# Performance work log

Hardware: AMD Instinct MI355X
Metric: run time of the kernel (lower is better)

## Reference

```python
import jax, jax.numpy as jnp
import numpy as np

H = 2048          # hidden_size
NH = 16           # num_heads
HD = H // NH      # head_dim = 128
B, S = 2, 2048


def setup_inputs() -> dict:
    key = jax.random.key(0)
    ks = jax.random.split(key, 9)
    sc_h = 1.0 / np.sqrt(H)
    x = jax.random.normal(ks[0], (B, S, H), dtype=jnp.float32)
    # torch nn.Linear weights are [out_features, in_features]
    Wq = jax.random.uniform(ks[1], (H, H), jnp.float32, -sc_h, sc_h)
    bq = jax.random.uniform(ks[2], (H,), jnp.float32, -sc_h, sc_h)
    Wk = jax.random.uniform(ks[3], (HD, H), jnp.float32, -sc_h, sc_h)
    bk = jax.random.uniform(ks[4], (HD,), jnp.float32, -sc_h, sc_h)
    Wv = jax.random.uniform(ks[5], (HD, H), jnp.float32, -sc_h, sc_h)
    bv = jax.random.uniform(ks[6], (HD,), jnp.float32, -sc_h, sc_h)
    Wo = jax.random.uniform(ks[7], (H, H), jnp.float32, -sc_h, sc_h)
    bo = jax.random.uniform(ks[8], (H,), jnp.float32, -sc_h, sc_h)
    return {"x": x, "Wq": Wq, "bq": bq, "Wk": Wk, "bk": bk,
            "Wv": Wv, "bv": bv, "Wo": Wo, "bo": bo}


def reference(x, Wq, bq, Wk, bk, Wv, bv, Wo, bo):
    b, s, _ = x.shape
    q = (jnp.einsum('bsh,oh->bso', x, Wq) + bq).reshape(b, s, NH, HD)
    q = q.transpose(0, 2, 1, 3)                      # [b, nh, s, hd]
    k = jnp.einsum('bsh,dh->bsd', x, Wk) + bk        # [b, s, hd] single KV head
    v = jnp.einsum('bsh,dh->bsd', x, Wv) + bv
    # shared-K attention scores: broadcast single K head across query heads
    attn = jnp.einsum('bnsd,btd->bnst', q, k) / jnp.sqrt(jnp.float32(HD))
    attn = jax.nn.softmax(attn, axis=-1)
    out = jnp.einsum('bnst,btd->bnsd', attn, v)      # [b, nh, s, hd]
    out = out.transpose(0, 2, 1, 3).reshape(b, s, H)
    return jnp.einsum('bsh,oh->bso', out, Wo) + bo
```

## Files before the change

### kernel.cpp

```cpp
#include <hip/hip_runtime.h>
#include <hip/hip_bf16.h>

typedef unsigned short u16;
typedef unsigned int u32;
typedef __bf16 bf16x8 __attribute__((ext_vector_type(8)));
typedef float f32x4 __attribute__((ext_vector_type(4)));

#define AS1 __attribute__((address_space(1)))
#define AS3 __attribute__((address_space(3)))

__device__ __forceinline__ u16 f2bf(float f) {
  unsigned u = __builtin_bit_cast(unsigned, f);
  u += 0x7FFFu + ((u >> 16) & 1u);
  return (u16)(u >> 16);
}

__device__ __forceinline__ void gload_lds16(const void* g, void* l) {
  __builtin_amdgcn_global_load_lds((AS1 void*)g, (AS3 void*)l, 16, 0, 0);
}

__global__ __launch_bounds__(256)
void cvt_all(const float* __restrict__ x,
             const float* __restrict__ Wq, const float* __restrict__ Wk,
             const float* __restrict__ Wv, const float* __restrict__ Wo,
             const float* __restrict__ bq, const float* __restrict__ bk,
             const float* __restrict__ bv,
             u16* __restrict__ xb, u16* __restrict__ wqkv, u16* __restrict__ wo,
             float* __restrict__ bias_a, float qs) {
  const long NX = 1048576, NQ = 524288, NK = 32768, NV = 32768, NO = 524288;
  const long NW = NX + NQ + NK + NV + NO;
  long i = (long)blockIdx.x * 256 + threadIdx.x;
  if (i >= NW) {
    int t = (int)(i - NW);
    if (t < 2048) bias_a[t] = bq[t] * qs;
    else if (t < 2176) bias_a[t] = bk[t - 2048];
    else if (t < 2304) bias_a[t] = bv[t - 2176];
    return;
  }
  const float* src;
  u16* dst;
  float s = 1.f;
  if (i < NX) { src = x + i * 8; dst = xb + i * 8; }
  else if (i < NX + NQ) { long j = i - NX; src = Wq + j * 8; dst = wqkv + j * 8; s = qs; }
  else if (i < NX + NQ + NK) { long j = i - NX - NQ; src = Wk + j * 8; dst = wqkv + 2048l * 2048 + j * 8; }
  else if (i < NX + NQ + NK + NV) { long j = i - NX - NQ - NK; src = Wv + j * 8; dst = wqkv + 2176l * 2048 + j * 8; }
  else { long j = i - NX - NQ - NK - NV; src = Wo + j * 8; dst = wo + j * 8; }
  float4 a = *(const float4*)src;
  float4 b = *(const float4*)(src + 4);
  u16 t[8] = {f2bf(a.x * s), f2bf(a.y * s), f2bf(a.z * s), f2bf(a.w * s),
              f2bf(b.x * s), f2bf(b.y * s), f2bf(b.z * s), f2bf(b.w * s)};
  *(uint4*)dst = *(const uint4*)t;
}

__global__ __launch_bounds__(256)
void gemm_qkv(const u16* __restrict__ A, const u16* __restrict__ B,
              const float* __restrict__ bias, u16* __restrict__ Cq,
              u16* __restrict__ Ck, u16* __restrict__ Cvt, int K)
{
  __shared__ u16 As[128 * 64];
  __shared__ u16 Bs[128 * 64];
  const int tid = threadIdx.x;
  const int wave = tid >> 6, lane = tid & 63;
  const int g = lane >> 4, r = lane & 15;
  const int wrow = (wave >> 1) * 64, wcol = (wave & 1) * 64;

  const int gx = gridDim.x;
  int lin = blockIdx.y * gx + blockIdx.x;
  const int cpx = (gx * gridDim.y) >> 3;
  lin = (lin & 7) * cpx + (lin >> 3);
  const long tM = (long)(lin / gx) * 128, tN = (long)(lin % gx) * 128;

  const int srow = (tid * 16) >> 7;
  const int scol = (tid & 7) * 8;

  f32x4 acc[4][4] = {};
  char* As3 = (char*)As;
  char* Bs3 = (char*)Bs;

  for (int kt = 0; kt < K; kt += 64) {
    __syncthreads();
#pragma unroll
    for (int p = 0; p < 4; p++) {
      const int row = p * 32 + srow;
      const int sc = scol ^ ((row & 7) << 3);
      gload_lds16(A + (tM + row) * K + kt + sc, As3 + p * 4096 + tid * 16);
      gload_lds16(B + (tN + row) * K + kt + sc, Bs3 + p * 4096 + tid * 16);
    }
    __syncthreads();

#pragma unroll
    for (int kk = 0; kk < 2; kk++) {
      bf16x8 a[4], b[4];
#pragma unroll
      for (int m = 0; m < 4; m++) {
        const int ra = wrow + m * 16 + r;
        a[m] = *(const bf16x8*)(As + ra * 64 + ((kk * 32 + g * 8) ^ ((ra & 7) << 3)));
      }
#pragma unroll
      for (int n = 0; n < 4; n++) {
        const int rb = wcol + n * 16 + r;
        b[n] = *(const bf16x8*)(Bs + rb * 64 + ((kk * 32 + g * 8) ^ ((rb & 7) << 3)));
      }
#pragma unroll
      for (int m = 0; m < 4; m++)
#pragma unroll
        for (int n = 0; n < 4; n++)
          acc[m][n] = __builtin_amdgcn_mfma_f32_16x16x32_bf16(a[m], b[n], acc[m][n], 0, 0, 0);
    }
  }

#pragma unroll
  for (int m = 0; m < 4; m++) {
    const long row0 = tM + wrow + m * 16 + g * 4;
#pragma unroll
    for (int n = 0; n < 4; n++) {
      const long col = tN + wcol + n * 16 + r;
      const float bb = bias[col];
      u16 vals[4];
#pragma unroll
      for (int q = 0; q < 4; q++) vals[q] = f2bf(acc[m][n][q] + bb);
      if (col < 2048) {
#pragma unroll
        for (int q = 0; q < 4; q++)
          Cq[(row0 + q) * 2048 + col] = vals[q];
      } else if (col < 2176) {
#pragma unroll
        for (int q = 0; q < 4; q++)
          Ck[(row0 + q) * 128 + (col - 2048)] = vals[q];
      } else {
        const long b2 = row0 >> 11;
        const long t0r = row0 & 2047;
        const int tl = (int)(t0r & 63);
        const int base = ((tl >> 5) & 1) * 32 + ((tl >> 2) & 3) * 8 + ((tl >> 4) & 1) * 4;
        u16* vp = Cvt + (b2 * 128 + (col - 2176)) * 2048 + (t0r >> 6) * 64;
        *(ushort4*)(vp + base) = *(const ushort4*)vals;
      }
    }
  }
}

__global__ __launch_bounds__(256)
void gemm_out(const u16* __restrict__ A, const u16* __restrict__ B,
              const float* __restrict__ bias, float* __restrict__ C,
              int N, int K)
{
  __shared__ u16 As[128 * 64];
  __shared__ u16 Bs[128 * 64];
  const int tid = threadIdx.x;
  const int wave = tid >> 6, lane = tid & 63;
  const int g = lane >> 4, r = lane & 15;
  const int wrow = (wave >> 1) * 64, wcol = (wave & 1) * 64;

  const int gx = gridDim.x;
  int lin = blockIdx.y * gx + blockIdx.x;
  const int cpx = (gx * gridDim.y) >> 3;
  lin = (lin & 7) * cpx + (lin >> 3);
  const long tM = (long)(lin / gx) * 128, tN = (long)(lin % gx) * 128;

  const int srow = (tid * 16) >> 7;
  const int scol = (tid & 7) * 8;

  f32x4 acc[4][4] = {};
  char* As3 = (char*)As;
  char* Bs3 = (char*)Bs;

  for (int kt = 0; kt < K; kt += 64) {
    __syncthreads();
#pragma unroll
    for (int p = 0; p < 4; p++) {
      const int row = p * 32 + srow;
      const int sc = scol ^ ((row & 7) << 3);
      gload_lds16(A + (tM + row) * K + kt + sc, As3 + p * 4096 + tid * 16);
      gload_lds16(B + (tN + row) * K + kt + sc, Bs3 + p * 4096 + tid * 16);
    }
    __syncthreads();

#pragma unroll
    for (int kk = 0; kk < 2; kk++) {
      bf16x8 a[4], b[4];
#pragma unroll
      for (int m = 0; m < 4; m++) {
        const int ra = wrow + m * 16 + r;
        a[m] = *(const bf16x8*)(As + ra * 64 + ((kk * 32 + g * 8) ^ ((ra & 7) << 3)));
      }
#pragma unroll
      for (int n = 0; n < 4; n++) {
        const int rb = wcol + n * 16 + r;
        b[n] = *(const bf16x8*)(Bs + rb * 64 + ((kk * 32 + g * 8) ^ ((rb & 7) << 3)));
      }
#pragma unroll
      for (int m = 0; m < 4; m++)
#pragma unroll
        for (int n = 0; n < 4; n++)
          acc[m][n] = __builtin_amdgcn_mfma_f32_16x16x32_bf16(a[m], b[n], acc[m][n], 0, 0, 0);
    }
  }

#pragma unroll
  for (int m = 0; m < 4; m++) {
    const long row0 = tM + wrow + m * 16 + g * 4;
#pragma unroll
    for (int n = 0; n < 4; n++) {
      const long col = tN + wcol + n * 16 + r;
      const float bb = bias[col];
#pragma unroll
      for (int q = 0; q < 4; q++)
        C[(row0 + q) * N + col] = acc[m][n][q] + bb;
    }
  }
}

__global__ __launch_bounds__(512, 2)
void attn_mqa15(const u16* __restrict__ Q, const u16* __restrict__ Kb,
                const u16* __restrict__ VT, u16* __restrict__ O)
{
  constexpr int S = 2048;
  const int bid = blockIdx.x;
  const int qt = bid & 7;
  const int head = (bid >> 3) & 15;
  const int b = bid >> 7;
  const int tid = threadIdx.x;
  const int wave = tid >> 6, lane = tid & 63;
  const int g = lane >> 4, r = lane & 15;

  __shared__ u16 Ks[2][64 * 128];
  __shared__ u16 VTs[2][128 * 64];

  bf16x8 qf[2][4];
#pragma unroll
  for (int qb = 0; qb < 2; qb++) {
    const u16* qp = Q + (long)(b * S + qt * 256 + qb * 128 + wave * 16 + r) * 2048
                      + head * 128 + g * 8;
#pragma unroll
    for (int ks = 0; ks < 4; ks++) qf[qb][ks] = *(const bf16x8*)(qp + ks * 32);
  }

  f32x4 oacc[2][8] = {};
  float lacc[2][4] = {};

  auto stageK = [&](int buf, int t0) {
    char* dst = (char*)Ks[buf];
#pragma unroll
    for (int p = 0; p < 2; p++) {
      int D = p * 8192 + wave * 1024 + lane * 16;
      int row = D >> 8;
      int col2 = (D & 255) ^ ((row & 7) << 4);
      gload_lds16(Kb + ((long)b * S + t0 + row) * 128 + (col2 >> 1), dst + D);
    }
  };
  auto stageV = [&](int buf, int t0) {
    char* dst = (char*)VTs[buf];
#pragma unroll
    for (int p = 0; p < 2; p++) {
      int D = p * 8192 + wave * 1024 + lane * 16;
      int row = D >> 7;
      int colb = (D & 127) ^ ((row & 7) << 4);
      gload_lds16(VT + ((long)b * 128 + row) * 2048 + t0 + (colb >> 1), dst + D);
    }
  };

  stageK(0, 0);
  stageV(0, 0);
  __syncthreads();

  for (int t0 = 0; t0 < S; t0 += 64) {
    const int cur = (t0 >> 6) & 1;
    const bool nxt = (t0 + 64) < S;

    if (nxt) { stageK(cur ^ 1, t0 + 64); stageV(cur ^ 1, t0 + 64); }

    char* Ks3 = (char*)Ks[cur];
    f32x4 st[2][4] = {};
    __builtin_amdgcn_s_setprio(1);
#pragma unroll
    for (int ks = 0; ks < 4; ks++) {
#pragma unroll
      for (int nf = 0; nf < 4; nf++) {
        const int trow = nf * 16 + r;
        const int col2 = (ks * 64 + g * 16) ^ ((trow & 7) << 4);
        bf16x8 kf = *(const bf16x8*)(Ks3 + trow * 256 + col2);
        st[0][nf] = __builtin_amdgcn_mfma_f32_16x16x32_bf16(kf, qf[0][ks], st[0][nf], 0, 0, 0);
        st[1][nf] = __builtin_amdgcn_mfma_f32_16x16x32_bf16(kf, qf[1][ks], st[1][nf], 0, 0, 0);
      }
    }
    __builtin_amdgcn_s_setprio(0);

    char* Vs3 = (char*)VTs[cur];
    bf16x8 vreg[2][8];
#pragma unroll
    for (int qb = 0; qb < 2; qb++) {
      bf16x8 pf[2];
#pragma unroll
      for (int ks = 0; ks < 2; ks++) {
        bf16x8 pv;
#pragma unroll
        for (int reg = 0; reg < 4; reg++) {
          float a = __builtin_amdgcn_exp2f(st[qb][ks * 2][reg]);
          float c = __builtin_amdgcn_exp2f(st[qb][ks * 2 + 1][reg]);
          lacc[qb][reg] += a + c;
          pv[reg] = (__bf16)a;
          pv[4 + reg] = (__bf16)c;
        }
        pf[ks] = pv;
      }
      __builtin_amdgcn_s_setprio(1);
#pragma unroll
      for (int ks = 0; ks < 2; ks++) {
#pragma unroll
        for (int dn = 0; dn < 8; dn++) {
          if (qb == 0) {
            const int d = dn * 16 + r;
            vreg[ks][dn] = *(const bf16x8*)(Vs3 + d * 128 +
                                            ((ks * 64 + g * 16) ^ ((d & 7) << 4)));
          }
          oacc[qb][dn] = __builtin_amdgcn_mfma_f32_16x16x32_bf16(vreg[ks][dn], pf[ks],
                                                                 oacc[qb][dn], 0, 0, 0);
        }
      }
      __builtin_amdgcn_s_setprio(0);
    }

    __syncthreads();
  }

  float lsum[2];
#pragma unroll
  for (int qb = 0; qb < 2; qb++) {
    lsum[qb] = (lacc[qb][0] + lacc[qb][1]) + (lacc[qb][2] + lacc[qb][3]);
    lsum[qb] += __shfl_xor(lsum[qb], 16);
    lsum[qb] += __shfl_xor(lsum[qb], 32);
  }

#pragma unroll
  for (int qb = 0; qb < 2; qb++) {
    const float inv = 1.f / lsum[qb];
    const long orow = (long)(b * S + qt * 256 + qb * 128 + wave * 16 + r);
#pragma unroll
    for (int dn = 0; dn < 8; dn++) {
      u16 pk4[4];
#pragma unroll
      for (int reg = 0; reg < 4; reg++) pk4[reg] = f2bf(oacc[qb][dn][reg] * inv);
      *(ushort4*)(O + orow * 2048 + head * 128 + dn * 16 + g * 4) =
          *(const ushort4*)pk4;
    }
  }
}

extern "C" void kernel_launch(void* const* d_in, const int* in_sizes, int n_in,
                              void* d_out, int out_size, void* d_ws, size_t ws_size,
                              hipStream_t stream) {
  const float* x  = (const float*)d_in[0];
  const float* Wq = (const float*)d_in[1];
  const float* bq = (const float*)d_in[2];
  const float* Wk = (const float*)d_in[3];
  const float* bk = (const float*)d_in[4];
  const float* Wv = (const float*)d_in[5];
  const float* bv = (const float*)d_in[6];
  const float* Wo = (const float*)d_in[7];
  const float* bo = (const float*)d_in[8];
  float* out = (float*)d_out;

  char* ws = (char*)d_ws;
  u16* x_bf     = (u16*)(ws + (0ul  << 20));
  u16* q_bf     = (u16*)(ws + (16ul << 20));
  u16* wqkv_bf  = (u16*)(ws + (32ul << 20));
  u16* wo_bf    = (u16*)(ws + (42ul << 20));
  u16* k_bf     = (u16*)(ws + (50ul << 20));
  u16* vt_bf    = (u16*)(ws + (51ul << 20));
  u16* attn_bf  = (u16*)(ws + (52ul << 20));
  float* bias_a = (float*)(ws + (68ul << 20));

  const float QS = 0.12751744f;

  cvt_all<<<8457, 256, 0, stream>>>(x, Wq, Wk, Wv, Wo, bq, bk, bv,
                                    x_bf, wqkv_bf, wo_bf, bias_a, QS);

  gemm_qkv<<<dim3(18, 32), 256, 0, stream>>>(
      x_bf, wqkv_bf, bias_a, q_bf, k_bf, vt_bf, 2048);
  attn_mqa15<<<256, 512, 0, stream>>>(q_bf, k_bf, vt_bf, attn_bf);
  gemm_out<<<dim3(16, 32), 256, 0, stream>>>(
      attn_bf, wo_bf, bo, out, 2048, 2048);
}
```

Measured before the change: 207.3 us.

## Split K/V projection from Q GEMM and compute it with split-K partials

The fused QKV GEMM grid of 18x32 tiles is replaced by a Q-only GEMM (16x32 tiles) plus a separate K/V GEMM that splits the 2048-long reduction into four chunks across blockIdx.z, writing fp32 partials. A finish kernel sums the partials, adds bias, converts to bf16 and writes K and the permuted V-transpose layout. The aim is to remove the tail wave caused by the 576-tile grid on the device's compute units and to give the narrow K/V output more parallelism. In exchange it adds two kernel launches and an extra fp32 round trip through memory for the partials, reusing the attention output buffer as scratch.

Result: faster. 194.2 us (-6.3%).

```diff
diff --git a/kernel.cpp b/kernel.cpp
--- a/kernel.cpp
+++ b/kernel.cpp
@@ -53,9 +53,8 @@
 }
 
 __global__ __launch_bounds__(256)
-void gemm_qkv(const u16* __restrict__ A, const u16* __restrict__ B,
-              const float* __restrict__ bias, u16* __restrict__ Cq,
-              u16* __restrict__ Ck, u16* __restrict__ Cvt, int K)
+void gemm_q(const u16* __restrict__ A, const u16* __restrict__ B,
+            const float* __restrict__ bias, u16* __restrict__ C, int K)
 {
   __shared__ u16 As[128 * 64];
   __shared__ u16 Bs[128 * 64];
@@ -116,26 +115,102 @@
     for (int n = 0; n < 4; n++) {
       const long col = tN + wcol + n * 16 + r;
       const float bb = bias[col];
-      u16 vals[4];
-#pragma unroll
-      for (int q = 0; q < 4; q++) vals[q] = f2bf(acc[m][n][q] + bb);
-      if (col < 2048) {
-#pragma unroll
-        for (int q = 0; q < 4; q++)
-          Cq[(row0 + q) * 2048 + col] = vals[q];
-      } else if (col < 2176) {
-#pragma unroll
-        for (int q = 0; q < 4; q++)
-          Ck[(row0 + q) * 128 + (col - 2048)] = vals[q];
-      } else {
-        const long b2 = row0 >> 11;
-        const long t0r = row0 & 2047;
-        const int tl = (int)(t0r & 63);
-        const int base = ((tl >> 5) & 1) * 32 + ((tl >> 2) & 3) * 8 + ((tl >> 4) & 1) * 4;
-        u16* vp = Cvt + (b2 * 128 + (col - 2176)) * 2048 + (t0r >> 6) * 64;
-        *(ushort4*)(vp + base) = *(const ushort4*)vals;
-      }
-    }
+#pragma unroll
+      for (int q = 0; q < 4; q++)
+        C[(row0 + q) * 2048 + col] = f2bf(acc[m][n][q] + bb);
+    }
+  }
+}
+
+__global__ __launch_bounds__(256)
+void gemm_kv(const u16* __restrict__ A, const u16* __restrict__ B,
+             float* __restrict__ P)
+{
+  __shared__ u16 As[128 * 64];
+  __shared__ u16 Bs[128 * 64];
+  const int tid = threadIdx.x;
+  const int wave = tid >> 6, lane = tid & 63;
+  const int g = lane >> 4, r = lane & 15;
+  const int wrow = (wave >> 1) * 64, wcol = (wave & 1) * 64;
+
+  const long tM = (long)blockIdx.y * 128;
+  const long tN = (long)blockIdx.x * 128;
+  const int kz = blockIdx.z;
+  const int K = 2048;
+
+  const int srow = (tid * 16) >> 7;
+  const int scol = (tid & 7) * 8;
+
+  f32x4 acc[4][4] = {};
+  char* As3 = (char*)As;
+  char* Bs3 = (char*)Bs;
+
+  for (int kt = kz * 512; kt < (kz + 1) * 512; kt += 64) {
+    __syncthreads();
+#pragma unroll
+    for (int p = 0; p < 4; p++) {
+      const int row = p * 32 + srow;
+      const int sc = scol ^ ((row & 7) << 3);
+      gload_lds16(A + (tM + row) * K + kt + sc, As3 + p * 4096 + tid * 16);
+      gload_lds16(B + (tN + row) * K + kt + sc, Bs3 + p * 4096 + tid * 16);
+    }
+    __syncthreads();
+
+#pragma unroll
+    for (int kk = 0; kk < 2; kk++) {
+      bf16x8 a[4], b[4];
+#pragma unroll
+      for (int m = 0; m < 4; m++) {
+        const int ra = wrow + m * 16 + r;
+        a[m] = *(const bf16x8*)(As + ra * 64 + ((kk * 32 + g * 8) ^ ((ra & 7) << 3)));
+      }
+#pragma unroll
+      for (int n = 0; n < 4; n++) {
+        const int rb = wcol + n * 16 + r;
+        b[n] = *(const bf16x8*)(Bs + rb * 64 + ((kk * 32 + g * 8) ^ ((rb & 7) << 3)));
+      }
+#pragma unroll
+      for (int m = 0; m < 4; m++)
+#pragma unroll
+        for (int n = 0; n < 4; n++)
+          acc[m][n] = __builtin_amdgcn_mfma_f32_16x16x32_bf16(a[m], b[n], acc[m][n], 0, 0, 0);
+    }
+  }
+
+  float* Pz = P + (long)kz * 4096 * 256;
+#pragma unroll
+  for (int m = 0; m < 4; m++) {
+    const long row0 = tM + wrow + m * 16 + g * 4;
+#pragma unroll
+    for (int n = 0; n < 4; n++) {
+      const long col = tN + wcol + n * 16 + r;
+#pragma unroll
+      for (int q = 0; q < 4; q++)
+        Pz[(row0 + q) * 256 + col] = acc[m][n][q];
+    }
+  }
+}
+
+__global__ __launch_bounds__(256)
+void kv_finish(const float* __restrict__ P, const float* __restrict__ bias,
+               u16* __restrict__ Ck, u16* __restrict__ Cvt)
+{
+  const long i = (long)blockIdx.x * 256 + threadIdx.x;
+  const int row = (int)(i >> 8);
+  const int col = (int)(i & 255);
+  const long NN = 4096l * 256;
+  float v = P[i] + P[i + NN] + P[i + 2 * NN] + P[i + 3 * NN] + bias[2048 + col];
+  u16 bv16 = f2bf(v);
+  if (col < 128) {
+    Ck[(long)row * 128 + col] = bv16;
+  } else {
+    const int d = col - 128;
+    const int b2 = row >> 11;
+    const int t = row & 2047;
+    const int tl = t & 63;
+    const int tlin = ((tl >> 5) & 1) * 32 + ((tl >> 2) & 3) * 8 +
+                     ((tl >> 4) & 1) * 4 + (tl & 3);
+    Cvt[((long)b2 * 128 + d) * 2048 + (t >> 6) * 64 + tlin] = bv16;
   }
 }
 
@@ -368,6 +443,7 @@
   u16* k_bf     = (u16*)(ws + (50ul << 20));
   u16* vt_bf    = (u16*)(ws + (51ul << 20));
   u16* attn_bf  = (u16*)(ws + (52ul << 20));
+  float* kvp    = (float*)(ws + (52ul << 20));
   float* bias_a = (float*)(ws + (68ul << 20));
 
   const float QS = 0.12751744f;
@@ -375,8 +451,10 @@
   cvt_all<<<8457, 256, 0, stream>>>(x, Wq, Wk, Wv, Wo, bq, bk, bv,
                                     x_bf, wqkv_bf, wo_bf, bias_a, QS);
 
-  gemm_qkv<<<dim3(18, 32), 256, 0, stream>>>(
-      x_bf, wqkv_bf, bias_a, q_bf, k_bf, vt_bf, 2048);
+  gemm_q<<<dim3(16, 32), 256, 0, stream>>>(x_bf, wqkv_bf, bias_a, q_bf, 2048);
+  gemm_kv<<<dim3(2, 32, 4), 256, 0, stream>>>(
+      x_bf, wqkv_bf + 2048l * 2048, kvp);
+  kv_finish<<<4096, 256, 0, stream>>>(kvp, bias_a, k_bf, vt_bf);
   attn_mqa15<<<256, 512, 0, stream>>>(q_bf, k_bf, vt_bf, attn_bf);
   gemm_out<<<dim3(16, 32), 256, 0, stream>>>(
       attn_bf, wo_bf, bo, out, 2048, 2048);
```
